# Performance work log

Measured on AMD Instinct MI355X. Metric: run time of the kernel, lower is better.

The kernel has to match this reference:

```python
import jax, jax.numpy as jnp
import numpy as np

B, NA, NMAX, NC = 32, 8400, 32, 80
TOPK, ALPHA, BETA, EPS, BG_IDX = 13, 1.0, 6.0, 1e-9, 80
IMG = 640.0


def _ciou(box1, box2, eps=1e-7):
    # box1: (b, nmax, 1, 4) xyxy, box2: (b, 1, na, 4) xyxy -> CIoU (b, nmax, na)
    b1_x1, b1_y1, b1_x2, b1_y2 = (box1[..., 0], box1[..., 1], box1[..., 2], box1[..., 3])
    b2_x1, b2_y1, b2_x2, b2_y2 = (box2[..., 0], box2[..., 1], box2[..., 2], box2[..., 3])
    inter = (jnp.minimum(b1_x2, b2_x2) - jnp.maximum(b1_x1, b2_x1)).clip(0) * \
            (jnp.minimum(b1_y2, b2_y2) - jnp.maximum(b1_y1, b2_y1)).clip(0)
    w1, h1 = b1_x2 - b1_x1, b1_y2 - b1_y1 + eps
    w2, h2 = b2_x2 - b2_x1, b2_y2 - b2_y1 + eps
    union = w1 * h1 + w2 * h2 - inter + eps
    iou = inter / union
    cw = jnp.maximum(b1_x2, b2_x2) - jnp.minimum(b1_x1, b2_x1)
    ch = jnp.maximum(b1_y2, b2_y2) - jnp.minimum(b1_y1, b2_y1)
    c2 = cw * cw + ch * ch + eps
    rho2 = ((b2_x1 + b2_x2 - b1_x1 - b1_x2) ** 2 + (b2_y1 + b2_y2 - b1_y1 - b1_y2) ** 2) / 4.0
    v = (4.0 / np.pi ** 2) * (jnp.arctan(w2 / h2) - jnp.arctan(w1 / h1)) ** 2
    alpha = jax.lax.stop_gradient(v / (v - iou + (1.0 + eps)))
    return iou - (rho2 / c2 + v * alpha)


def _rand_boxes(key, shape):
    # well-formed xyxy boxes inside a 640x640 image
    k1, k2 = jax.random.split(key)
    xy = jax.random.uniform(k1, shape[:-1] + (2,), jnp.float32) * (IMG - 64.0)
    wh = jax.random.uniform(k2, shape[:-1] + (2,), jnp.float32) * 56.0 + 8.0
    return jnp.concatenate([xy, xy + wh], axis=-1)


def setup_inputs() -> dict:
    key = jax.random.key(0)
    ks = jax.random.split(key, 6)
    pd_scores = jax.random.uniform(ks[0], (B, NA, NC), jnp.float32)
    pd_bboxes = _rand_boxes(ks[1], (B, NA, 4))
    anc_points = jax.random.uniform(ks[2], (NA, 2), jnp.float32) * IMG
    gt_labels = jax.random.randint(ks[3], (B, NMAX, 1), 0, NC, dtype=jnp.int32)
    gt_bboxes = _rand_boxes(ks[4], (B, NMAX, 4))
    mask_gt = jnp.ones((B, NMAX, 1), jnp.float32)
    return {"pd_scores": pd_scores, "pd_bboxes": pd_bboxes, "anc_points": anc_points,
            "gt_labels": gt_labels, "gt_bboxes": gt_bboxes, "mask_gt": mask_gt}


def reference(pd_scores, pd_bboxes, anc_points, gt_labels, gt_bboxes, mask_gt):
    b, na, nc = pd_scores.shape
    nmax = gt_bboxes.shape[1]
    # pairwise CIoU between every GT and every predicted box: (b, nmax, na)
    overlaps = _ciou(gt_bboxes[:, :, None, :], pd_bboxes[:, None, :, :])
    # gather predicted class score at each GT's label: (b, nmax, na)
    p = jnp.transpose(pd_scores, (0, 2, 1))                     # (b, nc, na)
    scores = jnp.take_along_axis(p, gt_labels.astype(jnp.int32), axis=1)
    align_metric = (scores ** ALPHA) * (overlaps ** BETA)
    # top-k anchors per GT along the anchor axis, scatter to a boolean mask
    _, topk_idx = jax.lax.top_k(align_metric, TOPK)             # (b, nmax, topk)
    bi = jnp.arange(b)[:, None, None]
    gi = jnp.arange(nmax)[None, :, None]
    mask_pos = jnp.zeros((b, nmax, na), bool).at[bi, gi, topk_idx].set(True)
    target_gt_idx = jnp.argmax(mask_pos, axis=1)                # (b, na)
    fg_mask = mask_pos.sum(axis=1) > 0                          # (b, na)
    # gather assigned GT label / box per anchor
    target_labels = jnp.take_along_axis(gt_labels[..., 0].astype(jnp.int32), target_gt_idx, axis=1)
    target_bboxes = jnp.take_along_axis(gt_bboxes, target_gt_idx[..., None], axis=1)  # (b, na, 4)
    target_scores = jax.nn.one_hot(target_labels, nc, dtype=jnp.float32) * fg_mask[..., None]
    target_labels = jnp.where(fg_mask, target_labels, BG_IDX)
    # normalize target scores by mean positive overlap per anchor, clamped to [0, 1]
    mpf = mask_pos.astype(overlaps.dtype)
    pos_overlaps = jnp.clip((overlaps * mpf).sum(axis=1) / (mpf.sum(axis=1) + EPS), 0.0, 1.0)
    target_scores = target_scores * pos_overlaps[..., None]
    return target_labels, target_bboxes, target_scores, fg_mask, target_gt_idx
```

## Files before the change

### kernel.cpp

```cpp
#include <hip/hip_runtime.h>
#include <math.h>

#define BATCH 32
#define NA 8400
#define NMAX 32
#define NC 80
#define TOPK 13
#define THREADS 256
#define NPT 33
#define TILE 64
#define SSTRIDE 81

#define OFF_BOX 268800
#define OFF_SCR 1344000
#define OFF_FG  22848000
#define OFF_TGT 23116800

__device__ __forceinline__ float ciou_f(float gx1, float gy1, float gx2, float gy2,
                                        float px1, float py1, float px2, float py2) {
    const float eps = 1e-7f;
    float iw = fmaxf(fminf(gx2, px2) - fmaxf(gx1, px1), 0.0f);
    float ih = fmaxf(fminf(gy2, py2) - fmaxf(gy1, py1), 0.0f);
    float inter = iw * ih;
    float w1 = gx2 - gx1, h1 = gy2 - gy1 + eps;
    float w2 = px2 - px1, h2 = py2 - py1 + eps;
    float uni = w1 * h1 + w2 * h2 - inter + eps;
    float iou = inter / uni;
    float cw = fmaxf(gx2, px2) - fminf(gx1, px1);
    float ch = fmaxf(gy2, py2) - fminf(gy1, py1);
    float c2 = cw * cw + ch * ch + eps;
    float dx = px1 + px2 - gx1 - gx2;
    float dy = py1 + py2 - gy1 - gy2;
    float rho2 = (dx * dx + dy * dy) / 4.0f;
    float dd = atanf(w2 / h2) - atanf(w1 / h1);
    float v = (float)(4.0 / (M_PI * M_PI)) * dd * dd;
    float alpha = v / (v - iou + (1.0f + eps));
    return iou - (rho2 / c2 + v * alpha);
}

__global__ __launch_bounds__(THREADS) void metric_kernel(
    const float* __restrict__ pd_scores, const float* __restrict__ pd_bboxes,
    const int* __restrict__ gt_labels, const float* __restrict__ gt_bboxes,
    float* __restrict__ met, unsigned int* __restrict__ mask) {
    const int b = blockIdx.y;
    const int abase = blockIdx.x * TILE;
    const int tid = threadIdx.x;
    const int na_tile = min(TILE, NA - abase);
    const float eps = 1e-7f;

    if (tid < na_tile) mask[(size_t)b * NA + abase + tid] = 0u;

    __shared__ float ssc[TILE][SSTRIDE];
    __shared__ float4 spbox[TILE];
    __shared__ float sgx1[NMAX], sgy1[NMAX], sgx2[NMAX], sgy2[NMAX];
    __shared__ float sa1[NMAX], sat1[NMAX];
    __shared__ int   slbl[NMAX];

    if (tid < NMAX) {
        float4 g = ((const float4*)gt_bboxes)[b * NMAX + tid];
        float w1 = g.z - g.x, h1 = g.w - g.y + eps;
        sgx1[tid] = g.x; sgy1[tid] = g.y; sgx2[tid] = g.z; sgy2[tid] = g.w;
        sa1[tid]  = w1 * h1;
        sat1[tid] = atanf(w1 / h1);
        slbl[tid] = gt_labels[b * NMAX + tid];
    } else if (tid >= 64 && tid < 64 + TILE) {
        int al = tid - 64;
        if (al < na_tile)
            spbox[al] = ((const float4*)pd_bboxes)[(size_t)b * NA + abase + al];
    }

    const float4* srec4 = (const float4*)(pd_scores + ((size_t)b * NA + abase) * NC);
    const int nf4 = na_tile * 20;
#pragma unroll
    for (int i = 0; i < 5; i++) {
        int f = tid + i * THREADS;
        if (f < nf4) {
            float4 v = srec4[f];
            int a = f / 20, c = f % 20;
            float* d = &ssc[a][c * 4];
            d[0] = v.x; d[1] = v.y; d[2] = v.z; d[3] = v.w;
        }
    }
    __syncthreads();

    const int al = tid & 63;
    const int gbase = (tid >> 6) * 8;
    if (al >= na_tile) return;

    float4 p = spbox[al];
    float w2 = p.z - p.x, h2 = p.w - p.y + eps;
    float a2  = w2 * h2;
    float at2 = atanf(w2 / h2);
    const size_t abs_a = (size_t)abase + al;

#pragma unroll
    for (int k = 0; k < 8; k++) {
        int gi = gbase + k;
        float gx1 = sgx1[gi], gy1 = sgy1[gi], gx2 = sgx2[gi], gy2 = sgy2[gi];
        float iw = fmaxf(fminf(gx2, p.z) - fmaxf(gx1, p.x), 0.0f);
        float ih = fmaxf(fminf(gy2, p.w) - fmaxf(gy1, p.y), 0.0f);
        float inter = iw * ih;
        float uni = sa1[gi] + a2 - inter + eps;
        float iou = inter / uni;
        float cw = fmaxf(gx2, p.z) - fminf(gx1, p.x);
        float ch = fmaxf(gy2, p.w) - fminf(gy1, p.y);
        float c2 = cw * cw + ch * ch + eps;
        float dx = p.x + p.z - gx1 - gx2;
        float dy = p.y + p.w - gy1 - gy2;
        float rho2 = (dx * dx + dy * dy) / 4.0f;
        float dd = at2 - sat1[gi];
        float v = (float)(4.0 / (M_PI * M_PI)) * dd * dd;
        float alpha = v / (v - iou + (1.0f + eps));
        float ov = iou - (rho2 / c2 + v * alpha);
        float sc = ssc[al][slbl[gi]];
        float ov2 = ov * ov;
        met[((size_t)b * NMAX + gi) * NA + abs_a] = sc * (ov2 * ov2 * ov2);
    }
}

__global__ __launch_bounds__(THREADS) void topk_kernel(
    const float* __restrict__ met, unsigned int* __restrict__ mask) {
    const int tid  = threadIdx.x;
    const int lane = tid & 63;
    const int w    = tid >> 6;
    const int bid  = blockIdx.x;
    const int b  = bid >> 5;
    const int gi = bid & 31;
    const float* mrow = met + ((size_t)b * NMAX + gi) * NA;

    float m[NPT];
#pragma unroll
    for (int j = 0; j < NPT; j++) {
        int a = j * THREADS + tid;
        m[j] = (a < NA) ? mrow[a] : -INFINITY;
    }

    float bv0 = -INFINITY, bv1 = -INFINITY;
    int   ba0 = 0x7FFFFFFF, ba1 = 0x7FFFFFFF;
#pragma unroll
    for (int j = 0; j < NPT; j++) {
        float v = m[j]; int a = j * THREADS + tid;
        bool beats0 = (v > bv0) || (v == bv0 && a < ba0);
        bool beats1 = (v > bv1) || (v == bv1 && a < ba1);
        if (beats0) { bv1 = bv0; ba1 = ba0; bv0 = v; ba0 = a; }
        else if (beats1) { bv1 = v; ba1 = a; }
    }
    bool valid1 = true;

    float rv = -INFINITY; int ra = 0x7FFFFFFF;
    for (int k = 0; k < TOPK; k++) {
        float v = bv0; int a = ba0;
#pragma unroll
        for (int s = 1; s < 64; s <<= 1) {
            float ov = __shfl_xor(v, s);
            int   oa = __shfl_xor(a, s);
            if (ov > v || (ov == v && oa < a)) { v = ov; a = oa; }
        }
        if (lane == k) { rv = v; ra = a; }
        if (ba0 == a) {
            if (valid1) { bv0 = bv1; ba0 = ba1; valid1 = false; }
            else {
                float nv = -INFINITY; int na_ = 0x7FFFFFFF;
#pragma unroll
                for (int j = 0; j < NPT; j++) {
                    float mv = m[j]; int ma = j * THREADS + tid;
                    bool below = (mv < v) || (mv == v && ma > a);
                    bool beats = (mv > nv) || (mv == nv && ma < na_);
                    if (below && beats) { nv = mv; na_ = ma; }
                }
                bv0 = nv; ba0 = na_;
            }
        }
    }

    __shared__ float lv[4 * TOPK];
    __shared__ int   la[4 * TOPK];
    if (lane < TOPK) { lv[w * TOPK + lane] = rv; la[w * TOPK + lane] = ra; }
    __syncthreads();

    if (w == 0) {
        float v = (lane < 4 * TOPK) ? lv[lane] : -INFINITY;
        int   a = (lane < 4 * TOPK) ? la[lane] : 0x7FFFFFFF;
        for (int k = 0; k < TOPK; k++) {
            float wv = v; int wa = a;
#pragma unroll
            for (int s = 1; s < 64; s <<= 1) {
                float ov = __shfl_xor(wv, s);
                int   oa = __shfl_xor(wa, s);
                if (ov > wv || (ov == wv && oa < wa)) { wv = ov; wa = oa; }
            }
            if (lane == 0) atomicOr(&mask[(size_t)b * NA + wa], 1u << gi);
            if (a == wa) { v = -INFINITY; a = 0x7FFFFFFF; }
        }
    }
}

__global__ __launch_bounds__(THREADS) void assign_score_kernel(
    const float* __restrict__ pd_bboxes, const int* __restrict__ gt_labels,
    const float* __restrict__ gt_bboxes, const unsigned int* __restrict__ mask,
    float* __restrict__ out) {
    const int tid = threadIdx.x;
    const int ab = blockIdx.x * 64;
    __shared__ float spo[64];
    __shared__ int   slb[64];

    if (tid < 64) {
        int idx = ab + tid;
        int b = idx / NA;
        unsigned msk = mask[idx];
        int tgt = msk ? (__ffs(msk) - 1) : 0;
        float4 gb = ((const float4*)gt_bboxes)[b * NMAX + tgt];
        int lbl = gt_labels[b * NMAX + tgt];
        float4 p = ((const float4*)pd_bboxes)[idx];

        float sum = 0.0f;
        int cnt = 0;
        unsigned mm = msk;
        while (mm) {
            int i = __ffs(mm) - 1;
            mm &= mm - 1;
            float4 g = ((const float4*)gt_bboxes)[b * NMAX + i];
            sum += ciou_f(g.x, g.y, g.z, g.w, p.x, p.y, p.z, p.w);
            cnt++;
        }
        float po = fminf(fmaxf(sum / ((float)cnt + 1e-9f), 0.0f), 1.0f);

        bool fg = (msk != 0);
        out[idx] = fg ? (float)lbl : 80.0f;
        ((float4*)(out + OFF_BOX))[idx] = gb;
        out[OFF_FG + idx]  = fg ? 1.0f : 0.0f;
        out[OFF_TGT + idx] = (float)tgt;
        spo[tid] = po;
        slb[tid] = fg ? lbl : -1;
    }
    __syncthreads();

    float4* obase = (float4*)(out + OFF_SCR + (size_t)ab * NC);
#pragma unroll
    for (int i = 0; i < 5; i++) {
        int f = tid + i * THREADS;
        int a = f / 20, c = f % 20;
        int lbl = slb[a];
        float4 z = make_float4(0.f, 0.f, 0.f, 0.f);
        if ((lbl >> 2) == c) ((float*)&z)[lbl & 3] = spo[a];
        obase[f] = z;
    }
}

extern "C" void kernel_launch(void* const* d_in, const int* in_sizes, int n_in,
                              void* d_out, int out_size, void* d_ws, size_t ws_size,
                              hipStream_t stream) {
    const float* pd_scores = (const float*)d_in[0];
    const float* pd_bboxes = (const float*)d_in[1];
    const int*   gt_labels = (const int*)d_in[3];
    const float* gt_bboxes = (const float*)d_in[4];

    float* out = (float*)d_out;
    unsigned int* mask = (unsigned int*)d_ws;
    float* met = out + OFF_SCR;

    dim3 g1((NA + TILE - 1) / TILE, BATCH);
    metric_kernel<<<g1, THREADS, 0, stream>>>(pd_scores, pd_bboxes,
                                              gt_labels, gt_bboxes, met, mask);
    topk_kernel<<<BATCH * NMAX, THREADS, 0, stream>>>(met, mask);
    assign_score_kernel<<<BATCH * NA / 64, THREADS, 0, stream>>>(
        pd_bboxes, gt_labels, gt_bboxes, mask, out);
}
```

Baseline: 95.42 us.

## Widen metric tile, batch score loads, and use nontemporal stores in assignment

Doubles the metric kernel anchor tile to 128, so each thread evaluates 16 GTs. Score rows are prefetched into registers before being written to shared memory, adding memory-level parallelism. The assignment kernel now uses all 256 threads per block for anchors and writes outputs with nontemporal stores to avoid polluting cache. This raises register pressure and halves the metric grid size, which may reduce occupancy.

```diff
diff --git a/kernel.cpp b/kernel.cpp
--- a/kernel.cpp
+++ b/kernel.cpp
@@ -8,13 +8,15 @@
 #define TOPK 13
 #define THREADS 256
 #define NPT 33
-#define TILE 64
+#define TILE 128
 #define SSTRIDE 81
 
 #define OFF_BOX 268800
 #define OFF_SCR 1344000
 #define OFF_FG  22848000
 #define OFF_TGT 23116800
+
+typedef float f32x4 __attribute__((ext_vector_type(4)));
 
 __device__ __forceinline__ float ciou_f(float gx1, float gy1, float gx2, float gy2,
                                         float px1, float py1, float px2, float py2) {
@@ -38,7 +40,7 @@
     return iou - (rho2 / c2 + v * alpha);
 }
 
-__global__ __launch_bounds__(THREADS) void metric_kernel(
+__global__ __launch_bounds__(THREADS, 2) void metric_kernel(
     const float* __restrict__ pd_scores, const float* __restrict__ pd_bboxes,
     const int* __restrict__ gt_labels, const float* __restrict__ gt_bboxes,
     float* __restrict__ met, unsigned int* __restrict__ mask) {
@@ -63,28 +65,33 @@
         sa1[tid]  = w1 * h1;
         sat1[tid] = atanf(w1 / h1);
         slbl[tid] = gt_labels[b * NMAX + tid];
-    } else if (tid >= 64 && tid < 64 + TILE) {
-        int al = tid - 64;
+    } else if (tid >= 128) {
+        int al = tid - 128;
         if (al < na_tile)
             spbox[al] = ((const float4*)pd_bboxes)[(size_t)b * NA + abase + al];
     }
 
     const float4* srec4 = (const float4*)(pd_scores + ((size_t)b * NA + abase) * NC);
     const int nf4 = na_tile * 20;
-#pragma unroll
-    for (int i = 0; i < 5; i++) {
+    float4 r[10];
+#pragma unroll
+    for (int i = 0; i < 10; i++) {
+        int f = tid + i * THREADS;
+        if (f < nf4) r[i] = srec4[f];
+    }
+#pragma unroll
+    for (int i = 0; i < 10; i++) {
         int f = tid + i * THREADS;
         if (f < nf4) {
-            float4 v = srec4[f];
             int a = f / 20, c = f % 20;
             float* d = &ssc[a][c * 4];
-            d[0] = v.x; d[1] = v.y; d[2] = v.z; d[3] = v.w;
+            d[0] = r[i].x; d[1] = r[i].y; d[2] = r[i].z; d[3] = r[i].w;
         }
     }
     __syncthreads();
 
-    const int al = tid & 63;
-    const int gbase = (tid >> 6) * 8;
+    const int al = tid & (TILE - 1);
+    const int gbase = (tid >> 7) * 16;
     if (al >= na_tile) return;
 
     float4 p = spbox[al];
@@ -94,7 +101,7 @@
     const size_t abs_a = (size_t)abase + al;
 
 #pragma unroll
-    for (int k = 0; k < 8; k++) {
+    for (int k = 0; k < 16; k++) {
         int gi = gbase + k;
         float gx1 = sgx1[gi], gy1 = sgy1[gi], gx2 = sgx2[gi], gy2 = sgy2[gi];
         float iw = fmaxf(fminf(gx2, p.z) - fmaxf(gx1, p.x), 0.0f);
@@ -200,12 +207,12 @@
     const float* __restrict__ gt_bboxes, const unsigned int* __restrict__ mask,
     float* __restrict__ out) {
     const int tid = threadIdx.x;
-    const int ab = blockIdx.x * 64;
-    __shared__ float spo[64];
-    __shared__ int   slb[64];
-
-    if (tid < 64) {
-        int idx = ab + tid;
+    const int ab = blockIdx.x * THREADS;
+    const int idx = ab + tid;
+    __shared__ float spo[THREADS];
+    __shared__ int   slb[THREADS];
+
+    {
         int b = idx / NA;
         unsigned msk = mask[idx];
         int tgt = msk ? (__ffs(msk) - 1) : 0;
@@ -226,24 +233,25 @@
         float po = fminf(fmaxf(sum / ((float)cnt + 1e-9f), 0.0f), 1.0f);
 
         bool fg = (msk != 0);
-        out[idx] = fg ? (float)lbl : 80.0f;
-        ((float4*)(out + OFF_BOX))[idx] = gb;
-        out[OFF_FG + idx]  = fg ? 1.0f : 0.0f;
-        out[OFF_TGT + idx] = (float)tgt;
+        __builtin_nontemporal_store(fg ? (float)lbl : 80.0f, &out[idx]);
+        f32x4 gbv = { gb.x, gb.y, gb.z, gb.w };
+        __builtin_nontemporal_store(gbv, (f32x4*)(out + OFF_BOX) + idx);
+        __builtin_nontemporal_store(fg ? 1.0f : 0.0f, &out[OFF_FG + idx]);
+        __builtin_nontemporal_store((float)tgt, &out[OFF_TGT + idx]);
         spo[tid] = po;
         slb[tid] = fg ? lbl : -1;
     }
     __syncthreads();
 
-    float4* obase = (float4*)(out + OFF_SCR + (size_t)ab * NC);
-#pragma unroll
-    for (int i = 0; i < 5; i++) {
+    f32x4* obase = (f32x4*)(out + OFF_SCR + (size_t)ab * NC);
+#pragma unroll
+    for (int i = 0; i < 20; i++) {
         int f = tid + i * THREADS;
         int a = f / 20, c = f % 20;
         int lbl = slb[a];
-        float4 z = make_float4(0.f, 0.f, 0.f, 0.f);
-        if ((lbl >> 2) == c) ((float*)&z)[lbl & 3] = spo[a];
-        obase[f] = z;
+        f32x4 z = { 0.f, 0.f, 0.f, 0.f };
+        if ((lbl >> 2) == c) z[lbl & 3] = spo[a];
+        __builtin_nontemporal_store(z, obase + f);
     }
 }
 
@@ -263,6 +271,6 @@
     metric_kernel<<<g1, THREADS, 0, stream>>>(pd_scores, pd_bboxes,
                                               gt_labels, gt_bboxes, met, mask);
     topk_kernel<<<BATCH * NMAX, THREADS, 0, stream>>>(met, mask);
-    assign_score_kernel<<<BATCH * NA / 64, THREADS, 0, stream>>>(
+    assign_score_kernel<<<BATCH * NA / THREADS, THREADS, 0, stream>>>(
         pd_bboxes, gt_labels, gt_bboxes, mask, out);
 }
```

Result: faster. 91.81 us (-3.8%).

## Enlarge metric tile, batch score loads, split assign/score kernels, move metric to workspace

Applied to the files above, without the earlier changes.

The metric kernel tile grows from 64 to 128 anchors, and each thread now covers 16 GTs instead of 8. The score-tile loads are batched into registers before the shared-memory stores to expose more memory-level parallelism. The assign/score kernel is split into a fully parallel per-anchor assign kernel and a separate score kernel, so the label/box writes no longer run on only 64 of 256 threads. The metric buffer moves to workspace when it fits, which avoids aliasing the score output region. In exchange the metric kernel uses more shared memory (about 41KB per block) and more registers, which can reduce occupancy, and the split adds one kernel launch.

```diff
diff --git a/kernel.cpp b/kernel.cpp
--- a/kernel.cpp
+++ b/kernel.cpp
@@ -8,7 +8,7 @@
 #define TOPK 13
 #define THREADS 256
 #define NPT 33
-#define TILE 64
+#define TILE 128
 #define SSTRIDE 81
 
 #define OFF_BOX 268800
@@ -38,7 +38,7 @@
     return iou - (rho2 / c2 + v * alpha);
 }
 
-__global__ __launch_bounds__(THREADS) void metric_kernel(
+__global__ __launch_bounds__(THREADS, 2) void metric_kernel(
     const float* __restrict__ pd_scores, const float* __restrict__ pd_bboxes,
     const int* __restrict__ gt_labels, const float* __restrict__ gt_bboxes,
     float* __restrict__ met, unsigned int* __restrict__ mask) {
@@ -63,28 +63,33 @@
         sa1[tid]  = w1 * h1;
         sat1[tid] = atanf(w1 / h1);
         slbl[tid] = gt_labels[b * NMAX + tid];
-    } else if (tid >= 64 && tid < 64 + TILE) {
-        int al = tid - 64;
+    } else if (tid >= 128) {
+        int al = tid - 128;
         if (al < na_tile)
             spbox[al] = ((const float4*)pd_bboxes)[(size_t)b * NA + abase + al];
     }
 
     const float4* srec4 = (const float4*)(pd_scores + ((size_t)b * NA + abase) * NC);
     const int nf4 = na_tile * 20;
-#pragma unroll
-    for (int i = 0; i < 5; i++) {
+    float4 r[10];
+#pragma unroll
+    for (int i = 0; i < 10; i++) {
+        int f = tid + i * THREADS;
+        if (f < nf4) r[i] = srec4[f];
+    }
+#pragma unroll
+    for (int i = 0; i < 10; i++) {
         int f = tid + i * THREADS;
         if (f < nf4) {
-            float4 v = srec4[f];
             int a = f / 20, c = f % 20;
             float* d = &ssc[a][c * 4];
-            d[0] = v.x; d[1] = v.y; d[2] = v.z; d[3] = v.w;
+            d[0] = r[i].x; d[1] = r[i].y; d[2] = r[i].z; d[3] = r[i].w;
         }
     }
     __syncthreads();
 
-    const int al = tid & 63;
-    const int gbase = (tid >> 6) * 8;
+    const int al = tid & (TILE - 1);
+    const int gbase = (tid >> 7) * 16;
     if (al >= na_tile) return;
 
     float4 p = spbox[al];
@@ -94,7 +99,7 @@
     const size_t abs_a = (size_t)abase + al;
 
 #pragma unroll
-    for (int k = 0; k < 8; k++) {
+    for (int k = 0; k < 16; k++) {
         int gi = gbase + k;
         float gx1 = sgx1[gi], gy1 = sgy1[gi], gx2 = sgx2[gi], gy2 = sgy2[gi];
         float iw = fmaxf(fminf(gx2, p.z) - fmaxf(gx1, p.x), 0.0f);
@@ -195,7 +200,26 @@
     }
 }
 
-__global__ __launch_bounds__(THREADS) void assign_score_kernel(
+__global__ __launch_bounds__(THREADS) void assign_kernel(
+    const float* __restrict__ pd_bboxes, const int* __restrict__ gt_labels,
+    const float* __restrict__ gt_bboxes, const unsigned int* __restrict__ mask,
+    float* __restrict__ out) {
+    int idx = blockIdx.x * THREADS + threadIdx.x;
+    int b = idx / NA;
+
+    unsigned msk = mask[idx];
+    int tgt = msk ? (__ffs(msk) - 1) : 0;
+    float4 gb = ((const float4*)gt_bboxes)[b * NMAX + tgt];
+    int lbl = gt_labels[b * NMAX + tgt];
+    bool fg = (msk != 0);
+
+    out[idx] = fg ? (float)lbl : 80.0f;
+    ((float4*)(out + OFF_BOX))[idx] = gb;
+    out[OFF_FG + idx]  = fg ? 1.0f : 0.0f;
+    out[OFF_TGT + idx] = (float)tgt;
+}
+
+__global__ __launch_bounds__(THREADS) void score_kernel(
     const float* __restrict__ pd_bboxes, const int* __restrict__ gt_labels,
     const float* __restrict__ gt_bboxes, const unsigned int* __restrict__ mask,
     float* __restrict__ out) {
@@ -208,11 +232,7 @@
         int idx = ab + tid;
         int b = idx / NA;
         unsigned msk = mask[idx];
-        int tgt = msk ? (__ffs(msk) - 1) : 0;
-        float4 gb = ((const float4*)gt_bboxes)[b * NMAX + tgt];
-        int lbl = gt_labels[b * NMAX + tgt];
         float4 p = ((const float4*)pd_bboxes)[idx];
-
         float sum = 0.0f;
         int cnt = 0;
         unsigned mm = msk;
@@ -224,14 +244,10 @@
             cnt++;
         }
         float po = fminf(fmaxf(sum / ((float)cnt + 1e-9f), 0.0f), 1.0f);
-
-        bool fg = (msk != 0);
-        out[idx] = fg ? (float)lbl : 80.0f;
-        ((float4*)(out + OFF_BOX))[idx] = gb;
-        out[OFF_FG + idx]  = fg ? 1.0f : 0.0f;
-        out[OFF_TGT + idx] = (float)tgt;
+        int tgt = msk ? (__ffs(msk) - 1) : 0;
+        int lbl = gt_labels[b * NMAX + tgt];
         spo[tid] = po;
-        slb[tid] = fg ? lbl : -1;
+        slb[tid] = msk ? lbl : -1;
     }
     __syncthreads();
 
@@ -257,12 +273,20 @@
 
     float* out = (float*)d_out;
     unsigned int* mask = (unsigned int*)d_ws;
-    float* met = out + OFF_SCR;
+
+    const size_t MASK_BYTES = (size_t)BATCH * NA * 4;
+    const size_t MET_BYTES  = (size_t)BATCH * NMAX * NA * 4;
+    const size_t met_off = (MASK_BYTES + 255) & ~(size_t)255;
+    float* met = (ws_size >= met_off + MET_BYTES)
+                   ? (float*)((char*)d_ws + met_off)
+                   : out + OFF_SCR;
 
     dim3 g1((NA + TILE - 1) / TILE, BATCH);
     metric_kernel<<<g1, THREADS, 0, stream>>>(pd_scores, pd_bboxes,
                                               gt_labels, gt_bboxes, met, mask);
     topk_kernel<<<BATCH * NMAX, THREADS, 0, stream>>>(met, mask);
-    assign_score_kernel<<<BATCH * NA / 64, THREADS, 0, stream>>>(
+    assign_kernel<<<BATCH * NA / THREADS, THREADS, 0, stream>>>(
         pd_bboxes, gt_labels, gt_bboxes, mask, out);
-}
+    score_kernel<<<BATCH * NA / 64, THREADS, 0, stream>>>(
+        pd_bboxes, gt_labels, gt_bboxes, mask, out);
+}
```

After: 98.42 us. +3.1%, slower.
